# Optimization experiments

Hardware: AMD Instinct MI355X
Metric: run time of the kernel (lower is better)

## Reference

```python
import jax, jax.numpy as jnp
import numpy as np

MAX_DEG = 6
N_ATOMS = 500000
BATCH = 1024
F_IN = 75
# atoms are sorted by degree (DeepChem ConvMol convention); counts for degree 0..6
DEG_COUNTS = [20000, 80000, 150000, 150000, 75000, 20000, 5000]
OFF = np.cumsum([0] + DEG_COUNTS)


def setup_inputs():
    key = jax.random.key(0)
    ks = jax.random.split(key, 20)

    def p(k, shape):
        return jax.random.normal(k, shape, jnp.float32) * 0.05

    inp = {}
    inp["atom_features"] = jax.random.normal(ks[0], (N_ATOMS, F_IN), jnp.float32)
    inp["membership"] = jax.random.randint(ks[1], (N_ATOMS,), 0, BATCH)
    for d in range(1, MAX_DEG + 1):
        inp[f"adj{d}"] = jax.random.randint(ks[1 + d], (DEG_COUNTS[d], d), 0, N_ATOMS)
    inp["gc1_Wn"] = p(ks[8], (MAX_DEG, F_IN, 64))
    inp["gc1_Ws"] = p(ks[9], (MAX_DEG + 1, F_IN, 64))
    inp["gc1_b"] = jnp.zeros((MAX_DEG + 1, 64), jnp.float32)
    inp["gc2_Wn"] = p(ks[10], (MAX_DEG, 64, 64))
    inp["gc2_Ws"] = p(ks[11], (MAX_DEG + 1, 64, 64))
    inp["gc2_b"] = jnp.zeros((MAX_DEG + 1, 64), jnp.float32)
    inp["bn1_gamma"] = jnp.ones((64,), jnp.float32)
    inp["bn1_beta"] = jnp.zeros((64,), jnp.float32)
    inp["bn1_mean"] = jnp.zeros((64,), jnp.float32)
    inp["bn1_var"] = jnp.ones((64,), jnp.float32)
    inp["bn3_gamma"] = jnp.ones((128,), jnp.float32)
    inp["bn3_beta"] = jnp.zeros((128,), jnp.float32)
    inp["bn3_mean"] = jnp.zeros((128,), jnp.float32)
    inp["bn3_var"] = jnp.ones((128,), jnp.float32)
    inp["d1_W"] = p(ks[12], (64, 128))
    inp["d1_b"] = jnp.zeros((128,), jnp.float32)
    inp["d2_W"] = p(ks[13], (256, 64))
    inp["d2_b"] = jnp.zeros((64,), jnp.float32)
    inp["d3_W"] = p(ks[14], (64, 1))
    inp["d3_b"] = jnp.zeros((1,), jnp.float32)
    return inp


def batch_norm(x, gamma, beta, mean, var, eps=1e-3):
    # keras BatchNormalization in inference mode (eps = keras default 1e-3)
    return gamma * (x - mean) * jax.lax.rsqrt(var + eps) + beta


def graph_conv(feat, adjs, Wn, Ws, b):
    # degree-0 atoms: self transform only
    outs = [feat[OFF[0]:OFF[1]] @ Ws[0] + b[0]]
    for d in range(1, MAX_DEG + 1):
        summed = feat[adjs[d - 1]].sum(axis=1)        # [n_d, F] neighbor-sum gather
        self_a = feat[OFF[d]:OFF[d + 1]]              # [n_d, F] atoms of degree d
        outs.append(summed @ Wn[d - 1] + self_a @ Ws[d] + b[d])
    return jnp.tanh(jnp.concatenate(outs, axis=0))


def graph_pool(feat, adjs):
    outs = [feat[OFF[0]:OFF[1]]]                      # degree-0: passthrough
    for d in range(1, MAX_DEG + 1):
        gathered = feat[adjs[d - 1]]                  # [n_d, d, F]
        self_a = feat[OFF[d]:OFF[d + 1]][:, None, :]  # [n_d, 1, F]
        outs.append(jnp.max(jnp.concatenate([self_a, gathered], axis=1), axis=1))
    return jnp.concatenate(outs, axis=0)


def graph_gather(feat, membership):
    s = jax.ops.segment_sum(feat, membership, num_segments=BATCH)
    m = jax.ops.segment_max(feat, membership, num_segments=BATCH)
    return jnp.tanh(jnp.concatenate([s, m], axis=1))  # [BATCH, 2F]


def reference(atom_features, membership, adj1, adj2, adj3, adj4, adj5, adj6,
              gc1_Wn, gc1_Ws, gc1_b, gc2_Wn, gc2_Ws, gc2_b,
              bn1_gamma, bn1_beta, bn1_mean, bn1_var,
              bn3_gamma, bn3_beta, bn3_mean, bn3_var,
              d1_W, d1_b, d2_W, d2_b, d3_W, d3_b):
    adjs = [adj1, adj2, adj3, adj4, adj5, adj6]
    h = graph_conv(atom_features, adjs, gc1_Wn, gc1_Ws, gc1_b)
    h = batch_norm(h, bn1_gamma, bn1_beta, bn1_mean, bn1_var)
    h = graph_pool(h, adjs)
    h = graph_conv(h, adjs, gc2_Wn, gc2_Ws, gc2_b)
    # NOTE: source code reuses self.batch_norm1 after gc2 (batch_norm2 is unused)
    h = batch_norm(h, bn1_gamma, bn1_beta, bn1_mean, bn1_var)
    h = graph_pool(h, adjs)
    h = jnp.tanh(h @ d1_W + d1_b)
    h = batch_norm(h, bn3_gamma, bn3_beta, bn3_mean, bn3_var)
    g = graph_gather(h, membership)                   # [BATCH, 256]
    g = jax.nn.sigmoid(g @ d2_W + d2_b)
    return g @ d3_W + d3_b                            # [BATCH, 1]
```

## Files before the change

### kernel.cpp

```cpp
#include <hip/hip_runtime.h>
#include <hip/hip_fp16.h>
#include <math.h>


struct AdjPtrs { const int* p[6]; };

typedef _Float16 f16x8 __attribute__((ext_vector_type(8)));
typedef float f32x4 __attribute__((ext_vector_type(4)));

#define SORT_NB 512
#define SORT_CHUNK 977

__device__ __forceinline__ float tanh_fast(float x) {
  float ax = fabsf(x);
  float r = __expf(-2.f * ax);
  float t = 1.f - 2.f * r * __builtin_amdgcn_rcpf(1.f + r);
  return copysignf(t, x);
}

__device__ __forceinline__ f16x8 max8(f16x8 a, f16x8 b) {
  #pragma unroll
  for (int i = 0; i < 8; i++) a[i] = (a[i] > b[i]) ? a[i] : b[i];
  return a;
}

__global__ __launch_bounds__(256) void k_hist_blk(const int* __restrict__ mem,
                                                  int* __restrict__ hist2) {
  __shared__ int lh[1024];
  int blk = blockIdx.x, tid = threadIdx.x;
  for (int i = tid; i < 1024; i += 256) lh[i] = 0;
  __syncthreads();
  int base = blk * SORT_CHUNK;
  int end = min(base + SORT_CHUNK, 500000);
  for (int i = base + tid; i < end; i += 256)
    atomicAdd(&lh[mem[i]], 1);
  __syncthreads();
  for (int i = tid; i < 1024; i += 256)
    hist2[blk * 1024 + i] = lh[i];
}

__global__ __launch_bounds__(512) void k_scan_blk(int* __restrict__ hist2,
                                                  int* __restrict__ hist) {
  __shared__ int sc[SORT_NB];
  int key = blockIdx.x, t = threadIdx.x;
  int v = hist2[t * 1024 + key];
  sc[t] = v;
  __syncthreads();
  for (int off = 1; off < SORT_NB; off <<= 1) {
    int u = (t >= off) ? sc[t - off] : 0;
    __syncthreads();
    sc[t] += u;
    __syncthreads();
  }
  hist2[t * 1024 + key] = sc[t] - v;
  if (t == SORT_NB - 1) hist[key] = sc[SORT_NB - 1];
}

__global__ __launch_bounds__(1024) void k_scan(const int* __restrict__ hist,
                                               int* __restrict__ start) {
  __shared__ int sc[1024];
  int t = threadIdx.x;
  int h = hist[t];
  sc[t] = h;
  __syncthreads();
  for (int off = 1; off < 1024; off <<= 1) {
    int v = (t >= off) ? sc[t - off] : 0;
    __syncthreads();
    sc[t] += v;
    __syncthreads();
  }
  start[t] = sc[t] - h;
}

__global__ __launch_bounds__(256) void k_scatter_blk(const int* __restrict__ mem,
                                                     const int* __restrict__ start,
                                                     const int* __restrict__ hist2,
                                                     int* __restrict__ list) {
  __shared__ int lh[1024];
  int blk = blockIdx.x, tid = threadIdx.x;
  for (int i = tid; i < 1024; i += 256) lh[i] = 0;
  __syncthreads();
  int base = blk * SORT_CHUNK;
  int end = min(base + SORT_CHUNK, 500000);
  for (int i = base + tid; i < end; i += 256) {
    int key = mem[i];
    int r = atomicAdd(&lh[key], 1);
    list[start[key] + hist2[blk * 1024 + key] + r] = i;
  }
}

__global__ __launch_bounds__(256) void k_prep(const float* __restrict__ feat,
                                              f16x8* __restrict__ out8) {
  int i = blockIdx.x * 256 + threadIdx.x;
  if (i >= 5000000) return;
  int a = i / 10;
  int jp = i - a * 10;
  int k0 = jp * 8;
  const float* src = feat + (size_t)a * 75 + k0;
  f16x8 v;
  #pragma unroll
  for (int e = 0; e < 8; e++) {
    float f = (k0 + e < 75) ? src[e] : 0.f;
    v[e] = (_Float16)f;
  }
  out8[i] = v;
}

__global__ __launch_bounds__(256) void k_prep_w(
    const float* __restrict__ Ws1, const float* __restrict__ Wn1,
    const float* __restrict__ Ws2, const float* __restrict__ Wn2,
    const float* __restrict__ d1W,
    __half* __restrict__ W1H, __half* __restrict__ W2H, __half* __restrict__ D1H) {
  int i = blockIdx.x * 256 + threadIdx.x;
  if (i < 71680) {
    int d = i / 10240, r = i - d * 10240;
    int j = r & 7, lane = (r >> 3) & 63, t = r >> 9;
    int n = (t & 3) * 16 + (lane & 15);
    int k = (t >> 2) * 32 + (lane >> 4) * 8 + j;
    float v = 0.f;
    if (k < 75) v = Ws1[d * 4800 + k * 64 + n];
    else if (k >= 80 && k < 155 && d > 0) v = Wn1[(d - 1) * 4800 + (k - 80) * 64 + n];
    W1H[i] = __float2half(v);
  } else if (i < 129024) {
    int i2 = i - 71680;
    int d = i2 / 8192, r = i2 - d * 8192;
    int j = r & 7, lane = (r >> 3) & 63, t = r >> 9;
    int n = (t & 3) * 16 + (lane & 15);
    int k = (t >> 2) * 32 + (lane >> 4) * 8 + j;
    float v = 0.f;
    if (k < 64) v = Ws2[d * 4096 + k * 64 + n];
    else if (d > 0) v = Wn2[(d - 1) * 4096 + (k - 64) * 64 + n];
    W2H[i2] = __float2half(v);
  } else {
    int i3 = i - 129024;
    int n = i3 >> 6, k = i3 & 63;
    float v = d1W[k * 128 + n];
    __half hi = __float2half(v);
    D1H[i3] = hi;
    D1H[8192 + i3] = __float2half(v - __half2float(hi));
  }
}

template<int FP, int NCH, int D>
__device__ __forceinline__ void gcm_run(
    const __half* __restrict__ featH, const int* __restrict__ adj_g,
    int abase, int na, const f16x8* __restrict__ Wf,
    const float* __restrict__ bias_d,
    const float* __restrict__ bng, const float* __restrict__ bnb,
    const float* __restrict__ bnm, const float* __restrict__ bnv,
    __half* __restrict__ out) {
  int tid = threadIdx.x;
  int lane = tid & 63, w = tid >> 6;
  int ln = lane & 15, q = lane >> 4;

  int ar[2][D > 0 ? D : 1];
  if (D > 0) {
    #pragma unroll
    for (int ms = 0; ms < 2; ms++) {
      int m = w * 32 + ms * 16 + ln;
      bool ok = (m < na);
      #pragma unroll
      for (int e = 0; e < D; e++)
        ar[ms][e] = ok ? adj_g[m * D + e] : 0;
    }
  }

  f32x4 acc[2][4];
  #pragma unroll
  for (int ns = 0; ns < 4; ns++) {
    float bj = bias_d[ns * 16 + ln];
    acc[0][ns] = (f32x4){bj, bj, bj, bj};
    acc[1][ns] = acc[0][ns];
  }

  #pragma unroll
  for (int c = 0; c < NCH; c++) {
    int ksg = c * 32 + q * 8;
    f16x8 af[2];
    #pragma unroll
    for (int ms = 0; ms < 2; ms++) {
      int m = w * 32 + ms * 16 + ln;
      if (ksg < FP) {
        af[ms] = *(const f16x8*)(featH + (size_t)(abase + m) * FP + ksg);
      } else if (D > 0) {
        int kb = ksg - FP;
        f16x8 v = *(const f16x8*)(featH + (size_t)ar[ms][0] * FP + kb);
        #pragma unroll
        for (int e = 1; e < D; e++) {
          f16x8 u = *(const f16x8*)(featH + (size_t)ar[ms][e] * FP + kb);
          v = v + u;
        }
        af[ms] = v;
      } else {
        af[ms] = (f16x8){};
      }
    }
    #pragma unroll
    for (int ns = 0; ns < 4; ns++) {
      f16x8 bf = Wf[(c * 4 + ns) * 64 + lane];
      acc[0][ns] = __builtin_amdgcn_mfma_f32_16x16x32_f16(af[0], bf, acc[0][ns], 0, 0, 0);
      acc[1][ns] = __builtin_amdgcn_mfma_f32_16x16x32_f16(af[1], bf, acc[1][ns], 0, 0, 0);
    }
  }

  #pragma unroll
  for (int ns = 0; ns < 4; ns++) {
    int j = ns * 16 + ln;
    float scv = bng[j] * rsqrtf(bnv[j] + 1e-3f);
    float shv = bnb[j] - bnm[j] * scv;
    #pragma unroll
    for (int ms = 0; ms < 2; ms++) {
      #pragma unroll
      for (int r = 0; r < 4; r++) {
        int atom = w * 32 + ms * 16 + q * 4 + r;
        if (atom < na)
          out[(size_t)(abase + atom) * 64 + j] =
              __float2half(tanh_fast(acc[ms][ns][r]) * scv + shv);
      }
    }
  }
}

template<int FP, int NCH>
__global__ __launch_bounds__(256, 5) void k_gcm(
    const __half* __restrict__ featH, AdjPtrs adjs,
    const __half* __restrict__ WtH, const float* __restrict__ bias,
    const float* __restrict__ bng, const float* __restrict__ bnb,
    const float* __restrict__ bnm, const float* __restrict__ bnv,
    __half* __restrict__ out) {
  int bid = blockIdx.x;
  int d, off, end, bloc;
  if      (bid < 157)  { d = 0; bloc = bid;        off = 0;      end = 20000;  }
  else if (bid < 782)  { d = 1; bloc = bid - 157;  off = 20000;  end = 100000; }
  else if (bid < 1954) { d = 2; bloc = bid - 782;  off = 100000; end = 250000; }
  else if (bid < 3126) { d = 3; bloc = bid - 1954; off = 250000; end = 400000; }
  else if (bid < 3712) { d = 4; bloc = bid - 3126; off = 400000; end = 475000; }
  else if (bid < 3869) { d = 5; bloc = bid - 3712; off = 475000; end = 495000; }
  else                 { d = 6; bloc = bid - 3869; off = 495000; end = 500000; }
  int abase = off + bloc * 128;
  int na = min(128, end - abase);
  const int* adj_g = (d > 0) ? adjs.p[d - 1] + (abase - off) * d : (const int*)0;
  const f16x8* Wf = (const f16x8*)WtH + d * (NCH * 4 * 64);
  const float* bias_d = bias + d * 64;

  switch (d) {
    case 0: gcm_run<FP, NCH, 0>(featH, adj_g, abase, na, Wf, bias_d, bng, bnb, bnm, bnv, out); break;
    case 1: gcm_run<FP, NCH, 1>(featH, adj_g, abase, na, Wf, bias_d, bng, bnb, bnm, bnv, out); break;
    case 2: gcm_run<FP, NCH, 2>(featH, adj_g, abase, na, Wf, bias_d, bng, bnb, bnm, bnv, out); break;
    case 3: gcm_run<FP, NCH, 3>(featH, adj_g, abase, na, Wf, bias_d, bng, bnb, bnm, bnv, out); break;
    case 4: gcm_run<FP, NCH, 4>(featH, adj_g, abase, na, Wf, bias_d, bng, bnb, bnm, bnv, out); break;
    case 5: gcm_run<FP, NCH, 5>(featH, adj_g, abase, na, Wf, bias_d, bng, bnb, bnm, bnv, out); break;
    default: gcm_run<FP, NCH, 6>(featH, adj_g, abase, na, Wf, bias_d, bng, bnb, bnm, bnv, out); break;
  }
}

template<int D>
__device__ __forceinline__ f16x8 pool_h_acc(const f16x8* __restrict__ in8,
                                            const int* __restrict__ ad, int sg, f16x8 v) {
  #pragma unroll
  for (int e = 0; e < D; e++) v = max8(v, in8[ad[e] * 8 + sg]);
  return v;
}

__global__ __launch_bounds__(256) void k_pool_h(const f16x8* __restrict__ in8, AdjPtrs adjs,
                                                f16x8* __restrict__ out8) {
  int t = blockIdx.x * 256 + threadIdx.x;
  int atom = t >> 3, sg = t & 7;
  int d, off;
  if      (atom < 20000)  { d = 0; off = 0;      }
  else if (atom < 100000) { d = 1; off = 20000;  }
  else if (atom < 250000) { d = 2; off = 100000; }
  else if (atom < 400000) { d = 3; off = 250000; }
  else if (atom < 475000) { d = 4; off = 400000; }
  else if (atom < 495000) { d = 5; off = 475000; }
  else                    { d = 6; off = 495000; }
  f16x8 v = in8[atom * 8 + sg];
  if (d > 0) {
    const int* ad = adjs.p[d - 1] + (atom - off) * d;
    switch (d) {
      case 1: v = pool_h_acc<1>(in8, ad, sg, v); break;
      case 2: v = pool_h_acc<2>(in8, ad, sg, v); break;
      case 3: v = pool_h_acc<3>(in8, ad, sg, v); break;
      case 4: v = pool_h_acc<4>(in8, ad, sg, v); break;
      case 5: v = pool_h_acc<5>(in8, ad, sg, v); break;
      default: v = pool_h_acc<6>(in8, ad, sg, v); break;
    }
  }
  out8[atom * 8 + sg] = v;
}

__global__ __launch_bounds__(256, 4) void k_dense1f(
    const __half* __restrict__ hD, const int* __restrict__ list,
    const int* __restrict__ start, const int* __restrict__ hist,
    const __half* __restrict__ D1H, const float* __restrict__ d1b,
    const float* __restrict__ g3, const float* __restrict__ b3,
    const float* __restrict__ m3, const float* __restrict__ v3,
    const float* __restrict__ W2, const float* __restrict__ b2,
    const float* __restrict__ W3, const float* __restrict__ b3d,
    float* __restrict__ out) {
  __shared__ float gr[256];
  __shared__ float part[4][64];
  int b = blockIdx.x, tid = threadIdx.x;
  int lane = tid & 63, w = tid >> 6;
  int ln = lane & 15, q = lane >> 4;
  int stt = start[b], cnt = hist[b];

  float bj[2], sc[2], sh[2];
  #pragma unroll
  for (int nf = 0; nf < 2; nf++) {
    int col = w * 32 + nf * 16 + ln;
    bj[nf] = d1b[col];
    sc[nf] = g3[col] * rsqrtf(v3[col] + 1e-3f);
    sh[nf] = b3[col] - m3[col] * sc[nf];
  }

  float sum[2] = {0.f, 0.f};
  float mx[2] = {-INFINITY, -INFINITY};

  for (int cb = 0; cb < cnt; cb += 64) {
    int nr = min(64, cnt - cb);
    int ridx[4];
    #pragma unroll
    for (int mf = 0; mf < 4; mf++) {
      int row = mf * 16 + ln;
      ridx[mf] = list[stt + cb + min(row, nr - 1)];
    }

    f32x4 acc[4][2];
    #pragma unroll
    for (int mf = 0; mf < 4; mf++)
      #pragma unroll
      for (int nf = 0; nf < 2; nf++) acc[mf][nf] = (f32x4){bj[nf], bj[nf], bj[nf], bj[nf]};

    #pragma unroll
    for (int hl = 1; hl >= 0; hl--) {
      #pragma unroll
      for (int ks = 0; ks < 2; ks++) {
        f16x8 af[4];
        #pragma unroll
        for (int mf = 0; mf < 4; mf++)
          af[mf] = *(const f16x8*)(hD + (size_t)ridx[mf] * 64 + ks * 32 + q * 8);
        #pragma unroll
        for (int nf = 0; nf < 2; nf++) {
          f16x8 bf = *(const f16x8*)(D1H + hl * 8192 +
                                     (w * 32 + nf * 16 + ln) * 64 + ks * 32 + q * 8);
          #pragma unroll
          for (int mf = 0; mf < 4; mf++)
            acc[mf][nf] = __builtin_amdgcn_mfma_f32_16x16x32_f16(af[mf], bf, acc[mf][nf], 0, 0, 0);
        }
      }
    }

    #pragma unroll
    for (int mf = 0; mf < 4; mf++) {
      #pragma unroll
      for (int nf = 0; nf < 2; nf++) {
        #pragma unroll
        for (int r = 0; r < 4; r++) {
          int row = mf * 16 + q * 4 + r;
          if (row < nr) {
            float v = tanh_fast(acc[mf][nf][r]) * sc[nf] + sh[nf];
            sum[nf] += v;
            mx[nf] = fmaxf(mx[nf], v);
          }
        }
      }
    }
  }

  #pragma unroll
  for (int nf = 0; nf < 2; nf++) {
    sum[nf] += __shfl_xor(sum[nf], 16);
    sum[nf] += __shfl_xor(sum[nf], 32);
    mx[nf] = fmaxf(mx[nf], __shfl_xor(mx[nf], 16));
    mx[nf] = fmaxf(mx[nf], __shfl_xor(mx[nf], 32));
  }
  if (q == 0) {
    #pragma unroll
    for (int nf = 0; nf < 2; nf++) {
      int col = w * 32 + nf * 16 + ln;
      gr[col] = tanh_fast(sum[nf]);
      gr[128 + col] = tanh_fast(mx[nf]);
    }
  }
  __syncthreads();

  int j = tid & 63, seg = tid >> 6;
  float a2 = 0.f;
  #pragma unroll 8
  for (int k = seg * 64; k < seg * 64 + 64; k++) a2 += gr[k] * W2[k * 64 + j];
  part[seg][j] = a2;
  __syncthreads();
  if (tid < 64) {
    float a = b2[j] + part[0][j] + part[1][j] + part[2][j] + part[3][j];
    float sg = 1.f / (1.f + expf(-a));
    float p = sg * W3[j];
    #pragma unroll
    for (int off = 32; off >= 1; off >>= 1) p += __shfl_xor(p, off);
    if (j == 0) out[b] = p + b3d[0];
  }
}

extern "C" void kernel_launch(void* const* d_in, const int* in_sizes, int n_in,
                              void* d_out, int out_size, void* d_ws, size_t ws_size,
                              hipStream_t stream) {
  const float* feat = (const float*)d_in[0];
  const int*   mem  = (const int*)d_in[1];
  AdjPtrs adjs;
  for (int i = 0; i < 6; i++) adjs.p[i] = (const int*)d_in[2 + i];
  const float* gc1_Wn = (const float*)d_in[8];
  const float* gc1_Ws = (const float*)d_in[9];
  const float* gc1_b  = (const float*)d_in[10];
  const float* gc2_Wn = (const float*)d_in[11];
  const float* gc2_Ws = (const float*)d_in[12];
  const float* gc2_b  = (const float*)d_in[13];
  const float* bn1g = (const float*)d_in[14];
  const float* bn1b = (const float*)d_in[15];
  const float* bn1m = (const float*)d_in[16];
  const float* bn1v = (const float*)d_in[17];
  const float* bn3g = (const float*)d_in[18];
  const float* bn3b = (const float*)d_in[19];
  const float* bn3m = (const float*)d_in[20];
  const float* bn3v = (const float*)d_in[21];
  const float* d1W = (const float*)d_in[22];
  const float* d1b = (const float*)d_in[23];
  const float* d2W = (const float*)d_in[24];
  const float* d2b = (const float*)d_in[25];
  const float* d3W = (const float*)d_in[26];
  const float* d3b = (const float*)d_in[27];
  float* out = (float*)d_out;

  char* w = (char*)d_ws;
  __half* featH = (__half*)(w);
  __half* hA    = (__half*)(w + 80000000LL);
  __half* hB    = (__half*)(w + 144000000LL);
  __half* hC    = (__half*)(w);
  __half* hD    = (__half*)(w + 80000000LL);
  __half* W1H   = (__half*)(w + 210000000LL);
  __half* W2H   = (__half*)(w + 210200000LL);
  __half* D1H   = (__half*)(w + 210330000LL);
  int* hist     = (int*)(w + 211600000LL);
  int* start    = (int*)(w + 211604096LL);
  int* list     = (int*)(w + 211612288LL);
  int* hist2    = (int*)(w + 144000000LL);

  k_hist_blk<<<SORT_NB, 256, 0, stream>>>(mem, hist2);
  k_scan_blk<<<1024, SORT_NB, 0, stream>>>(hist2, hist);
  k_scan<<<1, 1024, 0, stream>>>(hist, start);
  k_scatter_blk<<<SORT_NB, 256, 0, stream>>>(mem, start, hist2, list);

  k_prep<<<19532, 256, 0, stream>>>(feat, (f16x8*)featH);
  k_prep_w<<<536, 256, 0, stream>>>(gc1_Ws, gc1_Wn, gc2_Ws, gc2_Wn, d1W, W1H, W2H, D1H);

  k_gcm<80, 5><<<3909, 256, 0, stream>>>(featH, adjs, W1H, gc1_b,
                                         bn1g, bn1b, bn1m, bn1v, hA);
  k_pool_h<<<15625, 256, 0, stream>>>((const f16x8*)hA, adjs, (f16x8*)hB);
  k_gcm<64, 4><<<3909, 256, 0, stream>>>(hB, adjs, W2H, gc2_b,
                                         bn1g, bn1b, bn1m, bn1v, hC);
  k_pool_h<<<15625, 256, 0, stream>>>((const f16x8*)hC, adjs, (f16x8*)hD);
  k_dense1f<<<1024, 256, 0, stream>>>((const __half*)hD, list, start, hist, D1H, d1b,
                                      bn3g, bn3b, bn3m, bn3v,
                                      d2W, d2b, d3W, d3b, out);
}
```

Before: 601.8 us.

## Halve gcm tile to 64 atoms per block and prefetch gather indices in dense1f

The graph-conv MFMA kernel now gives each wave one 16-row m-fragment instead of two, so a block covers 64 atoms. The grid doubles and launch bounds rise to 8 blocks per CU. The aim is lower register pressure and more waves in flight to hide the latency of the irregular neighbor gathers. In the dense1 gather kernel, the next chunk's row indices are loaded while the current chunk computes, to overlap the index load latency. The cost is that each B-fragment weight load is reused across half as many MFMAs, and there are more blocks to schedule.

```diff
diff --git a/kernel.cpp b/kernel.cpp
--- a/kernel.cpp
+++ b/kernel.cpp
@@ -152,54 +152,44 @@
   int tid = threadIdx.x;
   int lane = tid & 63, w = tid >> 6;
   int ln = lane & 15, q = lane >> 4;
-
-  int ar[2][D > 0 ? D : 1];
+  int m = w * 16 + ln;
+
+  int ar[D > 0 ? D : 1];
   if (D > 0) {
-    #pragma unroll
-    for (int ms = 0; ms < 2; ms++) {
-      int m = w * 32 + ms * 16 + ln;
-      bool ok = (m < na);
-      #pragma unroll
-      for (int e = 0; e < D; e++)
-        ar[ms][e] = ok ? adj_g[m * D + e] : 0;
-    }
-  }
-
-  f32x4 acc[2][4];
+    bool ok = (m < na);
+    #pragma unroll
+    for (int e = 0; e < D; e++) ar[e] = ok ? adj_g[m * D + e] : 0;
+  }
+
+  f32x4 acc[4];
   #pragma unroll
   for (int ns = 0; ns < 4; ns++) {
     float bj = bias_d[ns * 16 + ln];
-    acc[0][ns] = (f32x4){bj, bj, bj, bj};
-    acc[1][ns] = acc[0][ns];
+    acc[ns] = (f32x4){bj, bj, bj, bj};
   }
 
   #pragma unroll
   for (int c = 0; c < NCH; c++) {
     int ksg = c * 32 + q * 8;
-    f16x8 af[2];
-    #pragma unroll
-    for (int ms = 0; ms < 2; ms++) {
-      int m = w * 32 + ms * 16 + ln;
-      if (ksg < FP) {
-        af[ms] = *(const f16x8*)(featH + (size_t)(abase + m) * FP + ksg);
-      } else if (D > 0) {
-        int kb = ksg - FP;
-        f16x8 v = *(const f16x8*)(featH + (size_t)ar[ms][0] * FP + kb);
-        #pragma unroll
-        for (int e = 1; e < D; e++) {
-          f16x8 u = *(const f16x8*)(featH + (size_t)ar[ms][e] * FP + kb);
-          v = v + u;
-        }
-        af[ms] = v;
-      } else {
-        af[ms] = (f16x8){};
+    f16x8 af;
+    if (ksg < FP) {
+      af = *(const f16x8*)(featH + (size_t)(abase + m) * FP + ksg);
+    } else if (D > 0) {
+      int kb = ksg - FP;
+      f16x8 v = *(const f16x8*)(featH + (size_t)ar[0] * FP + kb);
+      #pragma unroll
+      for (int e = 1; e < D; e++) {
+        f16x8 u = *(const f16x8*)(featH + (size_t)ar[e] * FP + kb);
+        v = v + u;
       }
+      af = v;
+    } else {
+      af = (f16x8){};
     }
     #pragma unroll
     for (int ns = 0; ns < 4; ns++) {
       f16x8 bf = Wf[(c * 4 + ns) * 64 + lane];
-      acc[0][ns] = __builtin_amdgcn_mfma_f32_16x16x32_f16(af[0], bf, acc[0][ns], 0, 0, 0);
-      acc[1][ns] = __builtin_amdgcn_mfma_f32_16x16x32_f16(af[1], bf, acc[1][ns], 0, 0, 0);
+      acc[ns] = __builtin_amdgcn_mfma_f32_16x16x32_f16(af, bf, acc[ns], 0, 0, 0);
     }
   }
 
@@ -209,20 +199,17 @@
     float scv = bng[j] * rsqrtf(bnv[j] + 1e-3f);
     float shv = bnb[j] - bnm[j] * scv;
     #pragma unroll
-    for (int ms = 0; ms < 2; ms++) {
-      #pragma unroll
-      for (int r = 0; r < 4; r++) {
-        int atom = w * 32 + ms * 16 + q * 4 + r;
-        if (atom < na)
-          out[(size_t)(abase + atom) * 64 + j] =
-              __float2half(tanh_fast(acc[ms][ns][r]) * scv + shv);
-      }
+    for (int r = 0; r < 4; r++) {
+      int atom = w * 16 + q * 4 + r;
+      if (atom < na)
+        out[(size_t)(abase + atom) * 64 + j] =
+            __float2half(tanh_fast(acc[ns][r]) * scv + shv);
     }
   }
 }
 
 template<int FP, int NCH>
-__global__ __launch_bounds__(256, 5) void k_gcm(
+__global__ __launch_bounds__(256, 8) void k_gcm(
     const __half* __restrict__ featH, AdjPtrs adjs,
     const __half* __restrict__ WtH, const float* __restrict__ bias,
     const float* __restrict__ bng, const float* __restrict__ bnb,
@@ -230,15 +217,15 @@
     __half* __restrict__ out) {
   int bid = blockIdx.x;
   int d, off, end, bloc;
-  if      (bid < 157)  { d = 0; bloc = bid;        off = 0;      end = 20000;  }
-  else if (bid < 782)  { d = 1; bloc = bid - 157;  off = 20000;  end = 100000; }
-  else if (bid < 1954) { d = 2; bloc = bid - 782;  off = 100000; end = 250000; }
-  else if (bid < 3126) { d = 3; bloc = bid - 1954; off = 250000; end = 400000; }
-  else if (bid < 3712) { d = 4; bloc = bid - 3126; off = 400000; end = 475000; }
-  else if (bid < 3869) { d = 5; bloc = bid - 3712; off = 475000; end = 495000; }
-  else                 { d = 6; bloc = bid - 3869; off = 495000; end = 500000; }
-  int abase = off + bloc * 128;
-  int na = min(128, end - abase);
+  if      (bid < 313)  { d = 0; bloc = bid;        off = 0;      end = 20000;  }
+  else if (bid < 1563) { d = 1; bloc = bid - 313;  off = 20000;  end = 100000; }
+  else if (bid < 3907) { d = 2; bloc = bid - 1563; off = 100000; end = 250000; }
+  else if (bid < 6251) { d = 3; bloc = bid - 3907; off = 250000; end = 400000; }
+  else if (bid < 7423) { d = 4; bloc = bid - 6251; off = 400000; end = 475000; }
+  else if (bid < 7736) { d = 5; bloc = bid - 7423; off = 475000; end = 495000; }
+  else                 { d = 6; bloc = bid - 7736; off = 495000; end = 500000; }
+  int abase = off + bloc * 64;
+  int na = min(64, end - abase);
   const int* adj_g = (d > 0) ? adjs.p[d - 1] + (abase - off) * d : (const int*)0;
   const f16x8* Wf = (const f16x8*)WtH + d * (NCH * 4 * 64);
   const float* bias_d = bias + d * 64;
@@ -317,13 +304,23 @@
   float sum[2] = {0.f, 0.f};
   float mx[2] = {-INFINITY, -INFINITY};
 
+  int ridx[4];
+  {
+    int nr0 = min(64, cnt);
+    #pragma unroll
+    for (int mf = 0; mf < 4; mf++)
+      ridx[mf] = list[stt + min(mf * 16 + ln, nr0 - 1)];
+  }
+
   for (int cb = 0; cb < cnt; cb += 64) {
     int nr = min(64, cnt - cb);
-    int ridx[4];
-    #pragma unroll
-    for (int mf = 0; mf < 4; mf++) {
-      int row = mf * 16 + ln;
-      ridx[mf] = list[stt + cb + min(row, nr - 1)];
+    int nridx[4];
+    int cb2 = cb + 64;
+    if (cb2 < cnt) {
+      int nr2 = min(64, cnt - cb2);
+      #pragma unroll
+      for (int mf = 0; mf < 4; mf++)
+        nridx[mf] = list[stt + cb2 + min(mf * 16 + ln, nr2 - 1)];
     }
 
     f32x4 acc[4][2];
@@ -365,6 +362,11 @@
           }
         }
       }
+    }
+
+    if (cb2 < cnt) {
+      #pragma unroll
+      for (int mf = 0; mf < 4; mf++) ridx[mf] = nridx[mf];
     }
   }
 
@@ -452,10 +454,10 @@
   k_prep<<<19532, 256, 0, stream>>>(feat, (f16x8*)featH);
   k_prep_w<<<536, 256, 0, stream>>>(gc1_Ws, gc1_Wn, gc2_Ws, gc2_Wn, d1W, W1H, W2H, D1H);
 
-  k_gcm<80, 5><<<3909, 256, 0, stream>>>(featH, adjs, W1H, gc1_b,
+  k_gcm<80, 5><<<7815, 256, 0, stream>>>(featH, adjs, W1H, gc1_b,
                                          bn1g, bn1b, bn1m, bn1v, hA);
   k_pool_h<<<15625, 256, 0, stream>>>((const f16x8*)hA, adjs, (f16x8*)hB);
-  k_gcm<64, 4><<<3909, 256, 0, stream>>>(hB, adjs, W2H, gc2_b,
+  k_gcm<64, 4><<<7815, 256, 0, stream>>>(hB, adjs, W2H, gc2_b,
                                          bn1g, bn1b, bn1m, bn1v, hC);
   k_pool_h<<<15625, 256, 0, stream>>>((const f16x8*)hC, adjs, (f16x8*)hD);
   k_dense1f<<<1024, 256, 0, stream>>>((const __half*)hD, list, start, hist, D1H, d1b,
```

New measurement: 607.1 us. About the same (+0.9%).
